# Performance work log

Measured on AMD Instinct MI355X. Metric: run time of the kernel, lower is better.

## Reference

```python
import jax, jax.numpy as jnp
import numpy as np

DIM = 128
NUM_TILES = 50000
NUM_PIECES = 25000
E_TT = 600000
E_PT = 400000


def _mean_aggregate(msgs, dst, num_dst):
    # msgs: [E, dim], dst: [E] int -> [num_dst, dim]
    agg = jax.ops.segment_sum(msgs, dst, num_segments=num_dst)
    cnt = jax.ops.segment_sum(jnp.ones((dst.shape[0], 1), msgs.dtype), dst,
                              num_segments=num_dst)
    return agg / jnp.maximum(cnt, 1.0)


def _linear(x, W, b):
    # torch nn.Linear: y = x @ W.T + b, W: [out, in]
    return x @ W.T + b


def setup_inputs() -> dict:
    key = jax.random.key(0)
    ks = jax.random.split(key, 20)
    s = 1.0 / np.sqrt(DIM)
    s2 = 1.0 / np.sqrt(2 * DIM)
    inp = {
        "tile_h": jax.random.normal(ks[0], (NUM_TILES, DIM), jnp.float32),
        "piece_h": jax.random.normal(ks[1], (NUM_PIECES, DIM), jnp.float32),
        "tile_src": jax.random.randint(ks[2], (E_PT,), 0, NUM_TILES),
        "piece_dst": jax.random.randint(ks[3], (E_PT,), 0, NUM_PIECES),
        "piece_src": jax.random.randint(ks[4], (E_PT,), 0, NUM_PIECES),
        "tile_dst": jax.random.randint(ks[5], (E_PT,), 0, NUM_TILES),
        "t_src": jax.random.randint(ks[6], (E_TT,), 0, NUM_TILES),
        "t_dst": jax.random.randint(ks[7], (E_TT,), 0, NUM_TILES),
        # weights: torch Linear layout [out_features, in_features]
        "W_t2p": jax.random.uniform(ks[8], (DIM, DIM), jnp.float32, -s, s),
        "b_t2p": jax.random.uniform(ks[9], (DIM,), jnp.float32, -s, s),
        "W_pu": jax.random.uniform(ks[10], (DIM, 2 * DIM), jnp.float32, -s2, s2),
        "b_pu": jax.random.uniform(ks[11], (DIM,), jnp.float32, -s2, s2),
        "W_p2t": jax.random.uniform(ks[12], (DIM, DIM), jnp.float32, -s, s),
        "b_p2t": jax.random.uniform(ks[13], (DIM,), jnp.float32, -s, s),
        "W_tup": jax.random.uniform(ks[14], (DIM, 2 * DIM), jnp.float32, -s2, s2),
        "b_tup": jax.random.uniform(ks[15], (DIM,), jnp.float32, -s2, s2),
        "W_t2t": jax.random.uniform(ks[16], (DIM, DIM), jnp.float32, -s, s),
        "b_t2t": jax.random.uniform(ks[17], (DIM,), jnp.float32, -s, s),
        "W_tut": jax.random.uniform(ks[18], (DIM, 2 * DIM), jnp.float32, -s2, s2),
        "b_tut": jax.random.uniform(ks[19], (DIM,), jnp.float32, -s2, s2),
    }
    return inp


def reference(tile_h, piece_h, tile_src, piece_dst, piece_src, tile_dst,
              t_src, t_dst,
              W_t2p, b_t2p, W_pu, b_pu, W_p2t, b_p2t,
              W_tup, b_tup, W_t2t, b_t2t, W_tut, b_tut):
    num_tiles = tile_h.shape[0]
    num_pieces = piece_h.shape[0]

    # Stage 1: tile -> piece
    msgs = _linear(tile_h[tile_src], W_t2p, b_t2p)          # [E_pt, dim]
    agg = _mean_aggregate(msgs, piece_dst, num_pieces)
    piece_h = jax.nn.relu(_linear(jnp.concatenate([piece_h, agg], axis=1), W_pu, b_pu))

    # Stage 2: piece -> tile
    msgs = _linear(piece_h[piece_src], W_p2t, b_p2t)        # [E_pt, dim]
    agg = _mean_aggregate(msgs, tile_dst, num_tiles)
    tile_h = jax.nn.relu(_linear(jnp.concatenate([tile_h, agg], axis=1), W_tup, b_tup))

    # Stage 3: tile -> tile
    msgs = _linear(tile_h[t_src], W_t2t, b_t2t)             # [E_tt, dim]
    agg = _mean_aggregate(msgs, t_dst, num_tiles)
    tile_h = jax.nn.relu(_linear(jnp.concatenate([tile_h, agg], axis=1), W_tut, b_tut))

    return (tile_h, piece_h)
```

## Files before the change

### kernel.cpp

```cpp
#include <hip/hip_runtime.h>
#include <hip/hip_bf16.h>

#define DIM 128
#define EPB 4096
#define BINS 512

typedef unsigned short u16;
typedef unsigned int u32;
typedef __attribute__((ext_vector_type(8))) short v8s;
typedef __attribute__((ext_vector_type(4))) float v4f;

__device__ __forceinline__ float bf2f(u16 u) {
    union { unsigned int i; float f; } v;
    v.i = ((unsigned int)u) << 16;
    return v.f;
}

__device__ __forceinline__ u16 f2bf(float f) {
    union { float f; unsigned int i; } v;
    v.f = f;
    unsigned int x = v.i;
    return (u16)((x + 0x7fffu + ((x >> 16) & 1u)) >> 16);
}

__device__ __forceinline__ uint4 pack8(float4 x0, float4 x1) {
    uint4 o;
    o.x = (u32)f2bf(x0.x) | ((u32)f2bf(x0.y) << 16);
    o.y = (u32)f2bf(x0.z) | ((u32)f2bf(x0.w) << 16);
    o.z = (u32)f2bf(x1.x) | ((u32)f2bf(x1.y) << 16);
    o.w = (u32)f2bf(x1.z) | ((u32)f2bf(x1.w) << 16);
    return o;
}

struct CvtArgs { const float* s[8]; u32 pfx[9]; };
__global__ __launch_bounds__(256) void cvt_and_count(
    CvtArgs a, u16* __restrict__ dst, int n8, int cvtB,
    const int* __restrict__ piece_dst, const int* __restrict__ tile_dst,
    const int* __restrict__ t_dst, int EPT, int ETT,
    int* __restrict__ counts, int NBLK)
{
    __shared__ int h[BINS];
    const int t = threadIdx.x;
    if (blockIdx.x < cvtB) {
        int g = blockIdx.x * 256 + t;
        if (g >= n8) return;
        u32 flat = (u32)g * 8;
        int seg = 0;
        #pragma unroll
        for (int i = 1; i < 8; ++i) if (flat >= a.pfx[i]) seg = i;
        const float4* fp = (const float4*)(a.s[seg] + (flat - a.pfx[seg]));
        *(uint4*)(dst + flat) = pack8(fp[0], fp[1]);
        return;
    }
    const int blk = blockIdx.x - cvtB;
    for (int d = t; d < BINS; d += 256) h[d] = 0;
    __syncthreads();
    const int ET = 2 * EPT + ETT;
    #pragma unroll 4
    for (int j = 0; j < EPB / 256; ++j) {
        int e = blk * EPB + j * 256 + t;
        if (e < ET) {
            int d;
            if (e < EPT)            d = (piece_dst[e] >> 9);
            else if (e < 2 * EPT)   d = 128 | (tile_dst[e - EPT] >> 9);
            else                    d = 256 | (t_dst[e - 2 * EPT] >> 9);
            atomicAdd(&h[d], 1);
        }
    }
    __syncthreads();
    for (int d = t; d < BINS; d += 256) counts[d * NBLK + blk] = h[d];
}

__global__ __launch_bounds__(256) void scan_gpart(const int* __restrict__ in,
                                                  int* __restrict__ out,
                                                  int* __restrict__ bsum, int n)
{
    __shared__ int ls[256];
    const int blk = blockIdx.x, t = threadIdx.x;
    const int base = blk * 2048;
    int v[8]; int s = 0;
    #pragma unroll
    for (int i = 0; i < 8; ++i) {
        int idx = base + t * 8 + i;
        v[i] = (idx < n) ? in[idx] : 0;
        s += v[i];
    }
    ls[t] = s;
    __syncthreads();
    #pragma unroll
    for (int o = 1; o < 256; o <<= 1) {
        int x = (t >= o) ? ls[t - o] : 0;
        __syncthreads();
        ls[t] += x;
        __syncthreads();
    }
    int run = (t == 0) ? 0 : ls[t - 1];
    #pragma unroll
    for (int i = 0; i < 8; ++i) {
        int idx = base + t * 8 + i;
        if (idx < n) out[idx] = run;
        run += v[i];
    }
    if (t == 255) bsum[blk] = ls[255];
}

__global__ __launch_bounds__(256) void scan_gfix(int* __restrict__ out,
                                                 const int* __restrict__ bsum, int n)
{
    __shared__ int off_s;
    const int blk = blockIdx.x, t = threadIdx.x;
    if (t == 0) {
        int o = 0;
        for (int i = 0; i < blk; ++i) o += bsum[i];
        off_s = o;
    }
    __syncthreads();
    const int off = off_s;
    const int base = blk * 2048;
    #pragma unroll
    for (int i = 0; i < 8; ++i) {
        int idx = base + t * 8 + i;
        if (idx < n) out[idx] += off;
    }
}

__global__ __launch_bounds__(256) void rs_scatter(
    const int* __restrict__ tile_src, const int* __restrict__ piece_dst,
    const int* __restrict__ piece_src, const int* __restrict__ tile_dst,
    const int* __restrict__ t_src, const int* __restrict__ t_dst,
    int EPT, int ETT,
    const int* __restrict__ countsS, int NBLK, int* __restrict__ T)
{
    __shared__ int p[BINS];
    const int t = threadIdx.x;
    const int blk = blockIdx.x;
    for (int d = t; d < BINS; d += 256) p[d] = countsS[d * NBLK + blk];
    __syncthreads();
    const int ET = 2 * EPT + ETT;
    #pragma unroll 4
    for (int j = 0; j < EPB / 256; ++j) {
        int e = blk * EPB + j * 256 + t;
        if (e < ET) {
            int dst, src, d;
            if (e < EPT) {
                dst = piece_dst[e]; src = tile_src[e]; d = dst >> 9;
            } else if (e < 2 * EPT) {
                int le = e - EPT;
                dst = tile_dst[le]; src = piece_src[le]; d = 128 | (dst >> 9);
            } else {
                int le = e - 2 * EPT;
                dst = t_dst[le]; src = t_src[le]; d = 256 | (dst >> 9);
            }
            int pos = atomicAdd(&p[d], 1);
            T[pos] = ((dst & 511) << 17) | src;
        }
    }
}

__global__ __launch_bounds__(256) void bucket_sort(
    const int* __restrict__ T, const int* __restrict__ countsS, int NBLK, int ET,
    int EPT, int ETT, int NP, int NT,
    int* __restrict__ el, int* __restrict__ rowptr)
{
    const int d = blockIdx.x;
    const int seg = d >> 7;
    if (seg > 2) return;
    const int dhi = d & 127;
    int Nseg, segOff, rb, Eseg;
    if (seg == 0)      { Nseg = NP; segOff = 0;       rb = 0;                 Eseg = EPT; }
    else if (seg == 1) { Nseg = NT; segOff = EPT;     rb = NP + 1;            Eseg = EPT; }
    else               { Nseg = NT; segOff = 2 * EPT; rb = NP + 1 + NT + 1;   Eseg = ETT; }

    const int bstart = countsS[d * NBLK];
    const int bend = (d < BINS - 1) ? countsS[(d + 1) * NBLK] : ET;

    __shared__ int hist[BINS];
    __shared__ int pos[BINS];
    __shared__ int ls[256];
    const int t = threadIdx.x;
    for (int i = t; i < BINS; i += 256) hist[i] = 0;
    __syncthreads();
    for (int j = bstart + t; j < bend; j += 256)
        atomicAdd(&hist[T[j] >> 17], 1);
    __syncthreads();
    int c0 = hist[2 * t], c1 = hist[2 * t + 1];
    ls[t] = c0 + c1;
    __syncthreads();
    #pragma unroll
    for (int o = 1; o < 256; o <<= 1) {
        int x = (t >= o) ? ls[t - o] : 0;
        __syncthreads();
        ls[t] += x;
        __syncthreads();
    }
    int ex = (t == 0) ? 0 : ls[t - 1];
    pos[2 * t]     = bstart + ex;
    pos[2 * t + 1] = bstart + ex + c0;
    __syncthreads();
    for (int i = t; i < BINS; i += 256) {
        int n = dhi * 512 + i;
        if (n < Nseg) rowptr[rb + n] = pos[i] - segOff;
    }
    if (t == 0 && dhi == ((Nseg - 1) >> 9)) rowptr[rb + Nseg] = Eseg;
    __syncthreads();
    for (int j = bstart + t; j < bend; j += 256) {
        int v = T[j];
        int p = atomicAdd(&pos[v >> 17], 1);
        el[p] = v & 0x1ffff;
    }
}

__global__ __launch_bounds__(256) void gather_mean_kernel(
    const u16* __restrict__ feat,
    const int* __restrict__ elist, const int* __restrict__ rowptr,
    int N, u16* __restrict__ meanA)
{
    int node = blockIdx.x * 16 + (threadIdx.x >> 4);
    int lane = threadIdx.x & 15;
    if (node >= N) return;
    int r0 = rowptr[node], r1 = rowptr[node + 1];
    float a0 = 0.f, a1 = 0.f, a2 = 0.f, a3 = 0.f;
    float a4 = 0.f, a5 = 0.f, a6 = 0.f, a7 = 0.f;
    int j = r0;
    for (; j + 4 <= r1; j += 4) {
        int s0 = elist[j], s1 = elist[j + 1], s2 = elist[j + 2], s3 = elist[j + 3];
        uint4 v0 = ((const uint4*)(feat + (size_t)s0 * DIM))[lane];
        uint4 v1 = ((const uint4*)(feat + (size_t)s1 * DIM))[lane];
        uint4 v2 = ((const uint4*)(feat + (size_t)s2 * DIM))[lane];
        uint4 v3 = ((const uint4*)(feat + (size_t)s3 * DIM))[lane];
        a0 += bf2f((u16)(v0.x & 0xffffu)); a1 += bf2f((u16)(v0.x >> 16));
        a2 += bf2f((u16)(v0.y & 0xffffu)); a3 += bf2f((u16)(v0.y >> 16));
        a4 += bf2f((u16)(v0.z & 0xffffu)); a5 += bf2f((u16)(v0.z >> 16));
        a6 += bf2f((u16)(v0.w & 0xffffu)); a7 += bf2f((u16)(v0.w >> 16));
        a0 += bf2f((u16)(v1.x & 0xffffu)); a1 += bf2f((u16)(v1.x >> 16));
        a2 += bf2f((u16)(v1.y & 0xffffu)); a3 += bf2f((u16)(v1.y >> 16));
        a4 += bf2f((u16)(v1.z & 0xffffu)); a5 += bf2f((u16)(v1.z >> 16));
        a6 += bf2f((u16)(v1.w & 0xffffu)); a7 += bf2f((u16)(v1.w >> 16));
        a0 += bf2f((u16)(v2.x & 0xffffu)); a1 += bf2f((u16)(v2.x >> 16));
        a2 += bf2f((u16)(v2.y & 0xffffu)); a3 += bf2f((u16)(v2.y >> 16));
        a4 += bf2f((u16)(v2.z & 0xffffu)); a5 += bf2f((u16)(v2.z >> 16));
        a6 += bf2f((u16)(v2.w & 0xffffu)); a7 += bf2f((u16)(v2.w >> 16));
        a0 += bf2f((u16)(v3.x & 0xffffu)); a1 += bf2f((u16)(v3.x >> 16));
        a2 += bf2f((u16)(v3.y & 0xffffu)); a3 += bf2f((u16)(v3.y >> 16));
        a4 += bf2f((u16)(v3.z & 0xffffu)); a5 += bf2f((u16)(v3.z >> 16));
        a6 += bf2f((u16)(v3.w & 0xffffu)); a7 += bf2f((u16)(v3.w >> 16));
    }
    for (; j < r1; ++j) {
        int s = elist[j];
        uint4 v = ((const uint4*)(feat + (size_t)s * DIM))[lane];
        a0 += bf2f((u16)(v.x & 0xffffu)); a1 += bf2f((u16)(v.x >> 16));
        a2 += bf2f((u16)(v.y & 0xffffu)); a3 += bf2f((u16)(v.y >> 16));
        a4 += bf2f((u16)(v.z & 0xffffu)); a5 += bf2f((u16)(v.z >> 16));
        a6 += bf2f((u16)(v.w & 0xffffu)); a7 += bf2f((u16)(v.w >> 16));
    }
    float sc = (r1 > r0) ? (1.f / (float)(r1 - r0)) : 0.f;
    uint4 o;
    o.x = (u32)f2bf(a0 * sc) | ((u32)f2bf(a1 * sc) << 16);
    o.y = (u32)f2bf(a2 * sc) | ((u32)f2bf(a3 * sc) << 16);
    o.z = (u32)f2bf(a4 * sc) | ((u32)f2bf(a5 * sc) << 16);
    o.w = (u32)f2bf(a6 * sc) | ((u32)f2bf(a7 * sc) << 16);
    ((uint4*)(meanA + (size_t)node * DIM))[lane] = o;
}

__global__ __launch_bounds__(256) void stage_fused(
    const u16* __restrict__ meanA, const int* __restrict__ rowptr,
    const u16* __restrict__ Wt, const float* __restrict__ bt,
    const u16* __restrict__ A1, const u16* __restrict__ Wu,
    const float* __restrict__ bu,
    u16* __restrict__ outC, float* __restrict__ outF, int N)
{
    __shared__ u16 Wl[128][136];
    __shared__ u16 Al[64][136];
    __shared__ u16 Bl[64][136];
    const int tid = threadIdx.x;
    const int nb = blockIdx.x * 64;
    const int wave = tid >> 6;
    const int lane = tid & 63;
    const int m = lane & 15;
    const int quad = lane >> 4;
    const int arow = wave * 16 + m;

    #pragma unroll
    for (int i = 0; i < 8; ++i) {
        int c = i * 256 + tid;
        int row = c >> 4;
        int c8 = (c & 15) * 8;
        *(uint4*)&Wl[row][c8] = *(const uint4*)(Wt + row * 128 + c8);
    }
    #pragma unroll
    for (int i = 0; i < 4; ++i) {
        int c = i * 256 + tid;
        int row = c >> 4;
        int c8 = (c & 15) * 8;
        int n = nb + row;
        uint4 v = {0u, 0u, 0u, 0u};
        if (n < N) v = *(const uint4*)(meanA + (size_t)n * DIM + c8);
        *(uint4*)&Al[row][c8] = v;
    }
    __syncthreads();

    v4f acct[8];
    #pragma unroll
    for (int t = 0; t < 8; ++t) acct[t] = (v4f){0.f, 0.f, 0.f, 0.f};
    #pragma unroll
    for (int k0 = 0; k0 < 128; k0 += 32) {
        v8s a = *(const v8s*)&Al[arow][k0 + quad * 8];
        #pragma unroll
        for (int t = 0; t < 8; ++t) {
            v8s b = *(const v8s*)&Wl[t * 16 + m][k0 + quad * 8];
            acct[t] = __builtin_amdgcn_mfma_f32_16x16x32_bf16(a, b, acct[t], 0, 0, 0);
        }
    }
    __syncthreads();

    {
        float btv[8];
        #pragma unroll
        for (int t = 0; t < 8; ++t) btv[t] = bt[t * 16 + m];
        #pragma unroll
        for (int r = 0; r < 4; ++r) {
            int n = nb + wave * 16 + quad * 4 + r;
            bool has = (n < N) && (rowptr[n + 1] > rowptr[n]);
            #pragma unroll
            for (int t = 0; t < 8; ++t) {
                float val = has ? (acct[t][r] + btv[t]) : 0.f;
                Bl[wave * 16 + quad * 4 + r][t * 16 + m] = f2bf(val);
            }
        }
    }
    #pragma unroll
    for (int i = 0; i < 8; ++i) {
        int c = i * 256 + tid;
        int row = c >> 4;
        int c8 = (c & 15) * 8;
        *(uint4*)&Wl[row][c8] = *(const uint4*)(Wu + row * 256 + c8);
    }
    #pragma unroll
    for (int i = 0; i < 4; ++i) {
        int c = i * 256 + tid;
        int row = c >> 4;
        int c8 = (c & 15) * 8;
        int n = nb + row;
        uint4 v = {0u, 0u, 0u, 0u};
        if (n < N) v = *(const uint4*)(A1 + (size_t)n * DIM + c8);
        *(uint4*)&Al[row][c8] = v;
    }
    __syncthreads();

    v4f accu[8];
    #pragma unroll
    for (int t = 0; t < 8; ++t) accu[t] = (v4f){0.f, 0.f, 0.f, 0.f};
    #pragma unroll
    for (int k0 = 0; k0 < 128; k0 += 32) {
        v8s a = *(const v8s*)&Al[arow][k0 + quad * 8];
        #pragma unroll
        for (int t = 0; t < 8; ++t) {
            v8s b = *(const v8s*)&Wl[t * 16 + m][k0 + quad * 8];
            accu[t] = __builtin_amdgcn_mfma_f32_16x16x32_bf16(a, b, accu[t], 0, 0, 0);
        }
    }
    __syncthreads();

    #pragma unroll
    for (int i = 0; i < 8; ++i) {
        int c = i * 256 + tid;
        int row = c >> 4;
        int c8 = (c & 15) * 8;
        *(uint4*)&Wl[row][c8] = *(const uint4*)(Wu + row * 256 + 128 + c8);
    }
    __syncthreads();

    #pragma unroll
    for (int k0 = 0; k0 < 128; k0 += 32) {
        v8s a = *(const v8s*)&Bl[arow][k0 + quad * 8];
        #pragma unroll
        for (int t = 0; t < 8; ++t) {
            v8s b = *(const v8s*)&Wl[t * 16 + m][k0 + quad * 8];
            accu[t] = __builtin_amdgcn_mfma_f32_16x16x32_bf16(a, b, accu[t], 0, 0, 0);
        }
    }

    float buv[8];
    #pragma unroll
    for (int t = 0; t < 8; ++t) buv[t] = bu[t * 16 + m];
    #pragma unroll
    for (int r = 0; r < 4; ++r) {
        int n = nb + wave * 16 + quad * 4 + r;
        if (n >= N) continue;
        #pragma unroll
        for (int t = 0; t < 8; ++t) {
            float val = accu[t][r] + buv[t];
            val = val > 0.f ? val : 0.f;
            if (outC) outC[(size_t)n * DIM + t * 16 + m] = f2bf(val);
            if (outF) outF[(size_t)n * DIM + t * 16 + m] = val;
        }
    }
}

extern "C" void kernel_launch(void* const* d_in, const int* in_sizes, int n_in,
                              void* d_out, int out_size, void* d_ws, size_t ws_size,
                              hipStream_t stream)
{
    const float* tile_h   = (const float*)d_in[0];
    const float* piece_h  = (const float*)d_in[1];
    const int* tile_src   = (const int*)d_in[2];
    const int* piece_dst  = (const int*)d_in[3];
    const int* piece_src  = (const int*)d_in[4];
    const int* tile_dst   = (const int*)d_in[5];
    const int* t_src      = (const int*)d_in[6];
    const int* t_dst      = (const int*)d_in[7];
    const float* b_t2p = (const float*)d_in[9];
    const float* b_pu  = (const float*)d_in[11];
    const float* b_p2t = (const float*)d_in[13];
    const float* b_tup = (const float*)d_in[15];
    const float* b_t2t = (const float*)d_in[17];
    const float* b_tut = (const float*)d_in[19];

    const int NT  = in_sizes[0] / DIM;
    const int NP  = in_sizes[1] / DIM;
    const int EPT = in_sizes[2];
    const int ETT = in_sizes[6];
    const int ET  = 2 * EPT + ETT;

    const int NBLK = (ET + EPB - 1) / EPB;
    const int n2 = BINS * NBLK;
    const int SB = (n2 + 2047) / 2048;

    char* ws = (char*)d_ws;
    size_t off = 0;
    int* counts = (int*)(ws + off);   off += (size_t)n2 * sizeof(int);
    off = (off + 255) & ~(size_t)255;
    int* countsS = (int*)(ws + off);  off += (size_t)n2 * sizeof(int);
    off = (off + 255) & ~(size_t)255;
    int* gbsum = (int*)(ws + off);    off += (size_t)((SB + 63) & ~63) * sizeof(int);
    off = (off + 255) & ~(size_t)255;
    int* rowptr = (int*)(ws + off);   off += (size_t)(NP + 2 * NT + 3) * sizeof(int);
    off = (off + 255) & ~(size_t)255;
    int* el = (int*)(ws + off);       off += (size_t)ET * sizeof(int);
    off = (off + 255) & ~(size_t)255;
    u16* A = (u16*)(ws + off);        off += (size_t)NT * DIM * sizeof(u16);
    off = (off + 255) & ~(size_t)255;
    u16* C = (u16*)(ws + off);        off += (size_t)NT * DIM * sizeof(u16);
    off = (off + 255) & ~(size_t)255;
    u16* arena = (u16*)(ws + off);

    int* T = (int*)A;

    const u32 nTh = (u32)NT * DIM, nPh = (u32)NP * DIM;
    u32 pfx[9];
    pfx[0] = 0;
    pfx[1] = nTh;
    pfx[2] = pfx[1] + nPh;
    pfx[3] = pfx[2] + 16384;
    pfx[4] = pfx[3] + 32768;
    pfx[5] = pfx[4] + 16384;
    pfx[6] = pfx[5] + 32768;
    pfx[7] = pfx[6] + 16384;
    pfx[8] = pfx[7] + 32768;

    u16* Th = arena + pfx[0];
    u16* Ph = arena + pfx[1];
    const u16* Wt2p = arena + pfx[2];
    const u16* Wpu  = arena + pfx[3];
    const u16* Wp2t = arena + pfx[4];
    const u16* Wtup = arena + pfx[5];
    const u16* Wt2t = arena + pfx[6];
    const u16* Wtut = arena + pfx[7];

    int* rp1 = rowptr;
    int* rp2 = rowptr + NP + 1;
    int* rp3 = rowptr + NP + 1 + NT + 1;
    int* el1 = el;
    int* el2 = el + EPT;
    int* el3 = el + 2 * EPT;

    float* out_tile  = (float*)d_out;
    float* out_piece = out_tile + (size_t)NT * DIM;

    dim3 blk(256);
    int n8 = (int)(pfx[8] / 8);
    const int cvtB = (n8 + 255) / 256;
    dim3 g_fat((unsigned)(cvtB + NBLK));
    dim3 g_rs((unsigned)NBLK);
    dim3 g_scan((unsigned)SB);
    dim3 g_bs((unsigned)BINS);
    dim3 g_gp((unsigned)((NP + 15) / 16));
    dim3 g_gt((unsigned)((NT + 15) / 16));
    dim3 g_np((unsigned)((NP + 63) / 64));
    dim3 g_nt((unsigned)((NT + 63) / 64));

    CvtArgs ca;
    ca.s[0] = tile_h; ca.s[1] = piece_h;
    ca.s[2] = (const float*)d_in[8];  ca.s[3] = (const float*)d_in[10];
    ca.s[4] = (const float*)d_in[12]; ca.s[5] = (const float*)d_in[14];
    ca.s[6] = (const float*)d_in[16]; ca.s[7] = (const float*)d_in[18];
    for (int i = 0; i < 9; ++i) ca.pfx[i] = pfx[i];
    hipLaunchKernelGGL(cvt_and_count, g_fat, blk, 0, stream,
                       ca, arena, n8, cvtB,
                       piece_dst, tile_dst, t_dst, EPT, ETT, counts, NBLK);

    hipLaunchKernelGGL(scan_gpart, g_scan, blk, 0, stream, counts, countsS, gbsum, n2);
    hipLaunchKernelGGL(scan_gfix, g_scan, blk, 0, stream, countsS, gbsum, n2);
    hipLaunchKernelGGL(rs_scatter, g_rs, blk, 0, stream,
                       tile_src, piece_dst, piece_src, tile_dst, t_src, t_dst,
                       EPT, ETT, countsS, NBLK, T);
    hipLaunchKernelGGL(bucket_sort, g_bs, blk, 0, stream,
                       T, countsS, NBLK, ET, EPT, ETT, NP, NT, el, rowptr);

    hipLaunchKernelGGL(gather_mean_kernel, g_gp, blk, 0, stream,
                       Th, el1, rp1, NP, A);
    hipLaunchKernelGGL(stage_fused, g_np, blk, 0, stream,
                       A, rp1, Wt2p, b_t2p, Ph, Wpu, b_pu, C, out_piece, NP);

    hipLaunchKernelGGL(gather_mean_kernel, g_gt, blk, 0, stream,
                       C, el2, rp2, NT, A);
    hipLaunchKernelGGL(stage_fused, g_nt, blk, 0, stream,
                       A, rp2, Wp2t, b_p2t, Th, Wtup, b_tup, C, (float*)nullptr, NT);

    hipLaunchKernelGGL(gather_mean_kernel, g_gt, blk, 0, stream,
                       C, el3, rp3, NT, A);
    hipLaunchKernelGGL(stage_fused, g_nt, blk, 0, stream,
                       A, rp3, Wt2t, b_t2t, C, Wtut, b_tut, (u16*)nullptr, out_tile, NT);
}
```

Before: 299.4 us.

## Fuse neighbor mean-gather into stage GEMM kernels and fold scan fixup into consumers

Removes the standalone gather_mean kernel. Each stage_fused block now gathers and averages neighbor features for its 64 rows straight into shared memory, and caches per-row degree in LDS instead of re-reading rowptr. This drops the intermediate mean-buffer write and read and three kernel launches. The scan_gfix kernel is also removed: rs_scatter and bucket_sort recompute the block-sum prefix locally, saving one more launch. The catch is that the latency-bound gather now runs inside a kernel with heavy LDS use and therefore lower occupancy.

New measurement: 323.6 us. 1.08x slower.

```diff
diff --git a/kernel.cpp b/kernel.cpp
--- a/kernel.cpp
+++ b/kernel.cpp
@@ -104,37 +104,29 @@
     if (t == 255) bsum[blk] = ls[255];
 }
 
-__global__ __launch_bounds__(256) void scan_gfix(int* __restrict__ out,
-                                                 const int* __restrict__ bsum, int n)
-{
-    __shared__ int off_s;
-    const int blk = blockIdx.x, t = threadIdx.x;
-    if (t == 0) {
-        int o = 0;
-        for (int i = 0; i < blk; ++i) o += bsum[i];
-        off_s = o;
-    }
-    __syncthreads();
-    const int off = off_s;
-    const int base = blk * 2048;
-    #pragma unroll
-    for (int i = 0; i < 8; ++i) {
-        int idx = base + t * 8 + i;
-        if (idx < n) out[idx] += off;
-    }
-}
-
 __global__ __launch_bounds__(256) void rs_scatter(
     const int* __restrict__ tile_src, const int* __restrict__ piece_dst,
     const int* __restrict__ piece_src, const int* __restrict__ tile_dst,
     const int* __restrict__ t_src, const int* __restrict__ t_dst,
     int EPT, int ETT,
-    const int* __restrict__ countsS, int NBLK, int* __restrict__ T)
+    const int* __restrict__ countsS, const int* __restrict__ bsum, int SB,
+    int NBLK, int* __restrict__ T)
 {
     __shared__ int p[BINS];
+    __shared__ int offp[128];
     const int t = threadIdx.x;
     const int blk = blockIdx.x;
-    for (int d = t; d < BINS; d += 256) p[d] = countsS[d * NBLK + blk];
+    if (t < SB) offp[t] = bsum[t];
+    __syncthreads();
+    if (t == 0) {
+        int run = 0;
+        for (int i = 0; i < SB; ++i) { int v = offp[i]; offp[i] = run; run += v; }
+    }
+    __syncthreads();
+    for (int d = t; d < BINS; d += 256) {
+        int idx = d * NBLK + blk;
+        p[d] = countsS[idx] + offp[idx >> 11];
+    }
     __syncthreads();
     const int ET = 2 * EPT + ETT;
     #pragma unroll 4
@@ -158,7 +150,8 @@
 }
 
 __global__ __launch_bounds__(256) void bucket_sort(
-    const int* __restrict__ T, const int* __restrict__ countsS, int NBLK, int ET,
+    const int* __restrict__ T, const int* __restrict__ countsS,
+    const int* __restrict__ bsum, int SB, int NBLK, int ET,
     int EPT, int ETT, int NP, int NT,
     int* __restrict__ el, int* __restrict__ rowptr)
 {
@@ -171,13 +164,24 @@
     else if (seg == 1) { Nseg = NT; segOff = EPT;     rb = NP + 1;            Eseg = EPT; }
     else               { Nseg = NT; segOff = 2 * EPT; rb = NP + 1 + NT + 1;   Eseg = ETT; }
 
-    const int bstart = countsS[d * NBLK];
-    const int bend = (d < BINS - 1) ? countsS[(d + 1) * NBLK] : ET;
-
     __shared__ int hist[BINS];
     __shared__ int pos[BINS];
     __shared__ int ls[256];
+    __shared__ int offp[128];
     const int t = threadIdx.x;
+    if (t < SB) offp[t] = bsum[t];
+    __syncthreads();
+    if (t == 0) {
+        int run = 0;
+        for (int i = 0; i < SB; ++i) { int v = offp[i]; offp[i] = run; run += v; }
+    }
+    __syncthreads();
+    int i0 = d * NBLK;
+    const int bstart = countsS[i0] + offp[i0 >> 11];
+    int bend;
+    if (d < BINS - 1) { int i1 = (d + 1) * NBLK; bend = countsS[i1] + offp[i1 >> 11]; }
+    else bend = ET;
+
     for (int i = t; i < BINS; i += 256) hist[i] = 0;
     __syncthreads();
     for (int j = bstart + t; j < bend; j += 256)
@@ -210,60 +214,15 @@
     }
 }
 
-__global__ __launch_bounds__(256) void gather_mean_kernel(
+#define ACC8(vv) do { \
+    af0 += bf2f((u16)((vv).x & 0xffffu)); af1 += bf2f((u16)((vv).x >> 16)); \
+    af2 += bf2f((u16)((vv).y & 0xffffu)); af3 += bf2f((u16)((vv).y >> 16)); \
+    af4 += bf2f((u16)((vv).z & 0xffffu)); af5 += bf2f((u16)((vv).z >> 16)); \
+    af6 += bf2f((u16)((vv).w & 0xffffu)); af7 += bf2f((u16)((vv).w >> 16)); } while (0)
+
+__global__ __launch_bounds__(256) void gather_stage_fused(
     const u16* __restrict__ feat,
-    const int* __restrict__ elist, const int* __restrict__ rowptr,
-    int N, u16* __restrict__ meanA)
-{
-    int node = blockIdx.x * 16 + (threadIdx.x >> 4);
-    int lane = threadIdx.x & 15;
-    if (node >= N) return;
-    int r0 = rowptr[node], r1 = rowptr[node + 1];
-    float a0 = 0.f, a1 = 0.f, a2 = 0.f, a3 = 0.f;
-    float a4 = 0.f, a5 = 0.f, a6 = 0.f, a7 = 0.f;
-    int j = r0;
-    for (; j + 4 <= r1; j += 4) {
-        int s0 = elist[j], s1 = elist[j + 1], s2 = elist[j + 2], s3 = elist[j + 3];
-        uint4 v0 = ((const uint4*)(feat + (size_t)s0 * DIM))[lane];
-        uint4 v1 = ((const uint4*)(feat + (size_t)s1 * DIM))[lane];
-        uint4 v2 = ((const uint4*)(feat + (size_t)s2 * DIM))[lane];
-        uint4 v3 = ((const uint4*)(feat + (size_t)s3 * DIM))[lane];
-        a0 += bf2f((u16)(v0.x & 0xffffu)); a1 += bf2f((u16)(v0.x >> 16));
-        a2 += bf2f((u16)(v0.y & 0xffffu)); a3 += bf2f((u16)(v0.y >> 16));
-        a4 += bf2f((u16)(v0.z & 0xffffu)); a5 += bf2f((u16)(v0.z >> 16));
-        a6 += bf2f((u16)(v0.w & 0xffffu)); a7 += bf2f((u16)(v0.w >> 16));
-        a0 += bf2f((u16)(v1.x & 0xffffu)); a1 += bf2f((u16)(v1.x >> 16));
-        a2 += bf2f((u16)(v1.y & 0xffffu)); a3 += bf2f((u16)(v1.y >> 16));
-        a4 += bf2f((u16)(v1.z & 0xffffu)); a5 += bf2f((u16)(v1.z >> 16));
-        a6 += bf2f((u16)(v1.w & 0xffffu)); a7 += bf2f((u16)(v1.w >> 16));
-        a0 += bf2f((u16)(v2.x & 0xffffu)); a1 += bf2f((u16)(v2.x >> 16));
-        a2 += bf2f((u16)(v2.y & 0xffffu)); a3 += bf2f((u16)(v2.y >> 16));
-        a4 += bf2f((u16)(v2.z & 0xffffu)); a5 += bf2f((u16)(v2.z >> 16));
-        a6 += bf2f((u16)(v2.w & 0xffffu)); a7 += bf2f((u16)(v2.w >> 16));
-        a0 += bf2f((u16)(v3.x & 0xffffu)); a1 += bf2f((u16)(v3.x >> 16));
-        a2 += bf2f((u16)(v3.y & 0xffffu)); a3 += bf2f((u16)(v3.y >> 16));
-        a4 += bf2f((u16)(v3.z & 0xffffu)); a5 += bf2f((u16)(v3.z >> 16));
-        a6 += bf2f((u16)(v3.w & 0xffffu)); a7 += bf2f((u16)(v3.w >> 16));
-    }
-    for (; j < r1; ++j) {
-        int s = elist[j];
-        uint4 v = ((const uint4*)(feat + (size_t)s * DIM))[lane];
-        a0 += bf2f((u16)(v.x & 0xffffu)); a1 += bf2f((u16)(v.x >> 16));
-        a2 += bf2f((u16)(v.y & 0xffffu)); a3 += bf2f((u16)(v.y >> 16));
-        a4 += bf2f((u16)(v.z & 0xffffu)); a5 += bf2f((u16)(v.z >> 16));
-        a6 += bf2f((u16)(v.w & 0xffffu)); a7 += bf2f((u16)(v.w >> 16));
-    }
-    float sc = (r1 > r0) ? (1.f / (float)(r1 - r0)) : 0.f;
-    uint4 o;
-    o.x = (u32)f2bf(a0 * sc) | ((u32)f2bf(a1 * sc) << 16);
-    o.y = (u32)f2bf(a2 * sc) | ((u32)f2bf(a3 * sc) << 16);
-    o.z = (u32)f2bf(a4 * sc) | ((u32)f2bf(a5 * sc) << 16);
-    o.w = (u32)f2bf(a6 * sc) | ((u32)f2bf(a7 * sc) << 16);
-    ((uint4*)(meanA + (size_t)node * DIM))[lane] = o;
-}
-
-__global__ __launch_bounds__(256) void stage_fused(
-    const u16* __restrict__ meanA, const int* __restrict__ rowptr,
+    const int* __restrict__ elist, const int* __restrict__ rowptr_seg,
     const u16* __restrict__ Wt, const float* __restrict__ bt,
     const u16* __restrict__ A1, const u16* __restrict__ Wu,
     const float* __restrict__ bu,
@@ -272,6 +231,7 @@
     __shared__ u16 Wl[128][136];
     __shared__ u16 Al[64][136];
     __shared__ u16 Bl[64][136];
+    __shared__ int degs[64];
     const int tid = threadIdx.x;
     const int nb = blockIdx.x * 64;
     const int wave = tid >> 6;
@@ -287,15 +247,41 @@
         int c8 = (c & 15) * 8;
         *(uint4*)&Wl[row][c8] = *(const uint4*)(Wt + row * 128 + c8);
     }
-    #pragma unroll
-    for (int i = 0; i < 4; ++i) {
-        int c = i * 256 + tid;
-        int row = c >> 4;
-        int c8 = (c & 15) * 8;
-        int n = nb + row;
-        uint4 v = {0u, 0u, 0u, 0u};
-        if (n < N) v = *(const uint4*)(meanA + (size_t)n * DIM + c8);
-        *(uint4*)&Al[row][c8] = v;
+
+    {
+        const int g = lane >> 4;
+        const int l16 = lane & 15;
+        #pragma unroll
+        for (int rr = 0; rr < 4; ++rr) {
+            int row = wave * 16 + rr * 4 + g;
+            int node = nb + row;
+            int r0 = 0, r1 = 0;
+            if (node < N) { r0 = rowptr_seg[node]; r1 = rowptr_seg[node + 1]; }
+            float af0 = 0.f, af1 = 0.f, af2 = 0.f, af3 = 0.f;
+            float af4 = 0.f, af5 = 0.f, af6 = 0.f, af7 = 0.f;
+            int j = r0;
+            for (; j + 4 <= r1; j += 4) {
+                int s0 = elist[j], s1 = elist[j + 1], s2 = elist[j + 2], s3 = elist[j + 3];
+                uint4 v0 = ((const uint4*)(feat + (size_t)s0 * DIM))[l16];
+                uint4 v1 = ((const uint4*)(feat + (size_t)s1 * DIM))[l16];
+                uint4 v2 = ((const uint4*)(feat + (size_t)s2 * DIM))[l16];
+                uint4 v3 = ((const uint4*)(feat + (size_t)s3 * DIM))[l16];
+                ACC8(v0); ACC8(v1); ACC8(v2); ACC8(v3);
+            }
+            for (; j < r1; ++j) {
+                int s = elist[j];
+                uint4 v = ((const uint4*)(feat + (size_t)s * DIM))[l16];
+                ACC8(v);
+            }
+            float sc = (r1 > r0) ? (1.f / (float)(r1 - r0)) : 0.f;
+            uint4 o;
+            o.x = (u32)f2bf(af0 * sc) | ((u32)f2bf(af1 * sc) << 16);
+            o.y = (u32)f2bf(af2 * sc) | ((u32)f2bf(af3 * sc) << 16);
+            o.z = (u32)f2bf(af4 * sc) | ((u32)f2bf(af5 * sc) << 16);
+            o.w = (u32)f2bf(af6 * sc) | ((u32)f2bf(af7 * sc) << 16);
+            *(uint4*)&Al[row][l16 * 8] = o;
+            if (l16 == 0) degs[row] = r1 - r0;
+        }
     }
     __syncthreads();
 
@@ -319,12 +305,13 @@
         for (int t = 0; t < 8; ++t) btv[t] = bt[t * 16 + m];
         #pragma unroll
         for (int r = 0; r < 4; ++r) {
-            int n = nb + wave * 16 + quad * 4 + r;
-            bool has = (n < N) && (rowptr[n + 1] > rowptr[n]);
+            int row = wave * 16 + quad * 4 + r;
+            int n = nb + row;
+            bool has = (n < N) && (degs[row] > 0);
             #pragma unroll
             for (int t = 0; t < 8; ++t) {
                 float val = has ? (acct[t][r] + btv[t]) : 0.f;
-                Bl[wave * 16 + quad * 4 + r][t * 16 + m] = f2bf(val);
+                Bl[row][t * 16 + m] = f2bf(val);
             }
         }
     }
@@ -438,13 +425,13 @@
     off = (off + 255) & ~(size_t)255;
     int* el = (int*)(ws + off);       off += (size_t)ET * sizeof(int);
     off = (off + 255) & ~(size_t)255;
-    u16* A = (u16*)(ws + off);        off += (size_t)NT * DIM * sizeof(u16);
-    off = (off + 255) & ~(size_t)255;
-    u16* C = (u16*)(ws + off);        off += (size_t)NT * DIM * sizeof(u16);
+    int* T = (int*)(ws + off);        off += (size_t)ET * sizeof(int);
+    off = (off + 255) & ~(size_t)255;
+    u16* Cp = (u16*)(ws + off);       off += (size_t)NP * DIM * sizeof(u16);
+    off = (off + 255) & ~(size_t)255;
+    u16* Ct = (u16*)(ws + off);       off += (size_t)NT * DIM * sizeof(u16);
     off = (off + 255) & ~(size_t)255;
     u16* arena = (u16*)(ws + off);
-
-    int* T = (int*)A;
 
     const u32 nTh = (u32)NT * DIM, nPh = (u32)NP * DIM;
     u32 pfx[9];
@@ -484,8 +471,6 @@
     dim3 g_rs((unsigned)NBLK);
     dim3 g_scan((unsigned)SB);
     dim3 g_bs((unsigned)BINS);
-    dim3 g_gp((unsigned)((NP + 15) / 16));
-    dim3 g_gt((unsigned)((NT + 15) / 16));
     dim3 g_np((unsigned)((NP + 63) / 64));
     dim3 g_nt((unsigned)((NT + 63) / 64));
 
@@ -500,25 +485,18 @@
                        piece_dst, tile_dst, t_dst, EPT, ETT, counts, NBLK);
 
     hipLaunchKernelGGL(scan_gpart, g_scan, blk, 0, stream, counts, countsS, gbsum, n2);
-    hipLaunchKernelGGL(scan_gfix, g_scan, blk, 0, stream, countsS, gbsum, n2);
     hipLaunchKernelGGL(rs_scatter, g_rs, blk, 0, stream,
                        tile_src, piece_dst, piece_src, tile_dst, t_src, t_dst,
-                       EPT, ETT, countsS, NBLK, T);
+                       EPT, ETT, countsS, gbsum, SB, NBLK, T);
     hipLaunchKernelGGL(bucket_sort, g_bs, blk, 0, stream,
-                       T, countsS, NBLK, ET, EPT, ETT, NP, NT, el, rowptr);
-
-    hipLaunchKernelGGL(gather_mean_kernel, g_gp, blk, 0, stream,
-                       Th, el1, rp1, NP, A);
-    hipLaunchKernelGGL(stage_fused, g_np, blk, 0, stream,
-                       A, rp1, Wt2p, b_t2p, Ph, Wpu, b_pu, C, out_piece, NP);
-
-    hipLaunchKernelGGL(gather_mean_kernel, g_gt, blk, 0, stream,
-                       C, el2, rp2, NT, A);
-    hipLaunchKernelGGL(stage_fused, g_nt, blk, 0, stream,
-                       A, rp2, Wp2t, b_p2t, Th, Wtup, b_tup, C, (float*)nullptr, NT);
-
-    hipLaunchKernelGGL(gather_mean_kernel, g_gt, blk, 0, stream,
-                       C, el3, rp3, NT, A);
-    hipLaunchKernelGGL(stage_fused, g_nt, blk, 0, stream,
-                       A, rp3, Wt2t, b_t2t, C, Wtut, b_tut, (u16*)nullptr, out_tile, NT);
-}
+                       T, countsS, gbsum, SB, NBLK, ET, EPT, ETT, NP, NT, el, rowptr);
+
+    hipLaunchKernelGGL(gather_stage_fused, g_np, blk, 0, stream,
+                       Th, el1, rp1, Wt2p, b_t2p, Ph, Wpu, b_pu, Cp, out_piece, NP);
+
+    hipLaunchKernelGGL(gather_stage_fused, g_nt, blk, 0, stream,
+                       Cp, el2, rp2, Wp2t, b_p2t, Th, Wtup, b_tup, Ct, (float*)nullptr, NT);
+
+    hipLaunchKernelGGL(gather_stage_fused, g_nt, blk, 0, stream,
+                       Ct, el3, rp3, Wt2t, b_t2t, Ct, Wtut, b_tut, (u16*)nullptr, out_tile, NT);
+}
```
